# Optimization experiments

Hardware: AMD Instinct MI355X
Metric: run time of the kernel (lower is better)

The kernel has to match this reference:

```python
import jax, jax.numpy as jnp
import numpy as np


def setup_inputs() -> dict:
    key = jax.random.key(0)
    ks = jax.random.split(key, 8)
    B, N, D, H = 8, 512, 64, 64
    user_embeddings = jax.random.normal(ks[0], (B, N, D), dtype=jnp.float32)
    past_lengths = jax.random.randint(ks[1], (B,), 0, N)
    valid_mask = jnp.ones((B, N), dtype=jnp.float32)
    # MLP params: Linear(4D -> H), PReLU (single slope), Linear(H -> 1)
    s1 = 1.0 / np.sqrt(4 * D)
    s2 = 1.0 / np.sqrt(H)
    W1 = jax.random.uniform(ks[2], (H, 4 * D), minval=-s1, maxval=s1, dtype=jnp.float32)
    b1 = jax.random.uniform(ks[3], (H,), minval=-s1, maxval=s1, dtype=jnp.float32)
    prelu_a = jnp.float32(0.25)
    W2 = jax.random.uniform(ks[4], (1, H), minval=-s2, maxval=s2, dtype=jnp.float32)
    b2 = jax.random.uniform(ks[5], (1,), minval=-s2, maxval=s2, dtype=jnp.float32)
    return {"past_lengths": past_lengths, "user_embeddings": user_embeddings,
            "valid_mask": valid_mask, "W1": W1, "b1": b1, "prelu_a": prelu_a,
            "W2": W2, "b2": b2}


def reference(past_lengths, user_embeddings, valid_mask, W1, b1, prelu_a, W2, b2):
    # DIN local activation attention with causal mask.
    # Original math: h = W1 @ concat(Q, K, Q-K, Q*K) + b1 per (q,k) pair.
    # Split W1 into its 4 D-sized blocks so the concat tensor [B,N,N,4D] is
    # never materialized; the pairwise hidden [B,N,N,H] is the only big buffer.
    B, N, D = user_embeddings.shape
    Wq, Wk, Wd, Wm = jnp.split(W1, 4, axis=1)  # each [H, D]
    x = user_embeddings
    # Q and (Q-K)'s +Q part -> per-query term; K and (Q-K)'s -K part -> per-key term
    hq = jnp.einsum('bqd,hd->bqh', x, Wq + Wd)          # [B,N,H]
    hk = jnp.einsum('bkd,hd->bkh', x, Wk - Wd)          # [B,N,H]
    hm = jnp.einsum('bqd,bkd,hd->bqkh', x, x, Wm)       # [B,N,N,H] (Q*K term)
    h = hq[:, :, None, :] + hk[:, None, :, :] + hm + b1
    h = jnp.where(h > 0, h, prelu_a * h)                # PReLU
    scores = jnp.einsum('bqkh,h->bqk', h, W2[0]) + b2[0]  # [B,N,N]
    causal = jnp.tril(jnp.ones((N, N), dtype=scores.dtype))
    scores = scores * causal[None, :, :]
    scores = scores * valid_mask[:, None, :]            # key-side padding mask
    encoded = jnp.einsum('bqk,bkd->bqd', scores, x)     # weighted sum (no softmax)
    return encoded
```

## Files before the change

### kernel.cpp

```cpp
#include <hip/hip_runtime.h>

#define NB 8
#define NN 512

#define WS_WMF 0
#define WS_HQ  4096
#define WS_BF  266240
#define WS_XE  528384

typedef float fx4 __attribute__((ext_vector_type(4)));
typedef short sx8 __attribute__((ext_vector_type(8)));
typedef int   ix4 __attribute__((ext_vector_type(4)));

static __device__ inline unsigned short f2bf(float f) {
    unsigned u = __float_as_uint(f);
    return (unsigned short)((u + 0x7FFFu + ((u >> 16) & 1u)) >> 16);
}

__global__ __launch_bounds__(256) void prep(const float* __restrict__ x,
                                            const float* __restrict__ vm,
                                            const float* __restrict__ W1,
                                            const float* __restrict__ b1,
                                            float* __restrict__ ws) {
    const int t = threadIdx.x;
    const int w = t >> 6, lane = t & 63;
    const int n = lane & 15, quad = lane >> 4;
    const int blk = blockIdx.x;
    const int b   = blk >> 3;
    const int tb  = (blk & 7) * 4;
    const int tile = tb + w;

    __shared__ unsigned short lwf[16 * 64 * 8];
    #pragma unroll
    for (int i = 0; i < 4; ++i) {
        int e = t + i * 256;
        int slot = e >> 6, L = e & 63;
        int isK = slot >> 3, ht = (slot >> 1) & 3, half = slot & 1;
        int nn = L & 15, qd = L >> 4;
        int h = ht * 16 + nn, dbase = half * 32 + qd * 8;
        unsigned short u[8];
        #pragma unroll
        for (int j = 0; j < 8; ++j) {
            int d = dbase + j;
            float wq = W1[h * 256 + d];
            float wk = W1[h * 256 + 64 + d];
            float wd = W1[h * 256 + 128 + d];
            u[j] = f2bf(isK ? (wk - wd) : (wq + wd));
        }
        uint4 o;
        o.x = (unsigned)u[0] | ((unsigned)u[1] << 16);
        o.y = (unsigned)u[2] | ((unsigned)u[3] << 16);
        o.z = (unsigned)u[4] | ((unsigned)u[5] << 16);
        o.w = (unsigned)u[6] | ((unsigned)u[7] << 16);
        ((uint4*)lwf)[e] = o;
    }

    if (blk < 2) {
        float* wmf = ws + WS_WMF;
        int e = blk * 256 + t;
        int slot = e >> 6, L = e & 63;
        int ht = slot >> 1, hf = slot & 1;
        int m = L & 15, qd = L >> 4;
        int h = ht * 16 + m;
        int dbase = hf * 32 + qd * 8;
        #pragma unroll
        for (int j = 0; j < 8; ++j)
            wmf[e * 8 + j] = W1[h * 256 + 192 + dbase + j];
    }
    __syncthreads();

    unsigned short* bfp = (unsigned short*)(ws + WS_BF);
    unsigned short* xep = (unsigned short*)(ws + WS_XE);
    float* hqp = ws + WS_HQ;

    sx8 ax0, ax1;
    {
        const float* xp = x + ((b * 512 + tile * 16 + n) * 64 + quad * 8);
        fx4 a0 = *(const fx4*)xp;
        fx4 a1 = *(const fx4*)(xp + 4);
        fx4 a2 = *(const fx4*)(xp + 32);
        fx4 a3 = *(const fx4*)(xp + 36);
        #pragma unroll
        for (int j = 0; j < 4; ++j) {
            ax0[j] = (short)f2bf(a0[j]); ax0[4 + j] = (short)f2bf(a1[j]);
            ax1[j] = (short)f2bf(a2[j]); ax1[4 + j] = (short)f2bf(a3[j]);
        }
    }

    *(uint4*)(bfp + ((((b * 32 + tile) * 4 + 0) * 64 + lane) << 3)) =
        __builtin_bit_cast(uint4, ax0);
    *(uint4*)(bfp + ((((b * 32 + tile) * 4 + 1) * 64 + lane) << 3)) =
        __builtin_bit_cast(uint4, ax1);

    #pragma unroll
    for (int ht = 0; ht < 4; ++ht) {
        sx8 bq0 = *(const sx8*)(lwf + ((ht * 2 + 0) << 9) + lane * 8);
        sx8 bq1 = *(const sx8*)(lwf + ((ht * 2 + 1) << 9) + lane * 8);
        sx8 bk0 = *(const sx8*)(lwf + ((8 + ht * 2 + 0) << 9) + lane * 8);
        sx8 bk1 = *(const sx8*)(lwf + ((8 + ht * 2 + 1) << 9) + lane * 8);

        float bv = b1[ht * 16 + n];
        fx4 hqa = (fx4){bv, bv, bv, bv};
        hqa = __builtin_amdgcn_mfma_f32_16x16x32_bf16(ax0, bq0, hqa, 0, 0, 0);
        hqa = __builtin_amdgcn_mfma_f32_16x16x32_bf16(ax1, bq1, hqa, 0, 0, 0);
        fx4 hka = (fx4){0.f, 0.f, 0.f, 0.f};
        hka = __builtin_amdgcn_mfma_f32_16x16x32_bf16(ax0, bk0, hka, 0, 0, 0);
        hka = __builtin_amdgcn_mfma_f32_16x16x32_bf16(ax1, bk1, hka, 0, 0, 0);

        #pragma unroll
        for (int r = 0; r < 4; ++r)
            hqp[(b * 512 + tile * 16 + quad * 4 + r) * 64 + ht * 16 + n] = hqa[r];

        int c   = 2 + (ht >> 1);
        int qd2 = (((ht & 1) * 16 + n) >> 3);
        int j   = n & 7;
        #pragma unroll
        for (int r = 0; r < 4; ++r) {
            int nn = quad * 4 + r;
            bfp[((((b * 32 + tile) * 4 + c) * 64 + (qd2 * 16 + nn)) << 3) + j] =
                f2bf(hka[r]);
        }
    }

    #pragma unroll 1
    for (int i = 0; i < 4; ++i) {
        int t5 = tb + i;
        int c32 = t5 >> 1, half = t5 & 1;
        int nt = t >> 6, r = t & 63;
        int L = half * 32 + (r & 31);
        int j0 = (r >> 5) * 4;
        int qd3 = L >> 4, nn3 = L & 15;
        unsigned short u[4];
        #pragma unroll
        for (int ii = 0; ii < 4; ++ii) {
            int key = c32 * 32 + qd3 * 8 + j0 + ii;
            float v = x[(b * 512 + key) * 64 + nt * 16 + nn3] * vm[b * 512 + key];
            u[ii] = f2bf(v);
        }
        uint2 o;
        o.x = (unsigned)u[0] | ((unsigned)u[1] << 16);
        o.y = (unsigned)u[2] | ((unsigned)u[3] << 16);
        *(uint2*)(xep + (((((b * 16 + c32) * 4 + nt) * 64 + L) << 3) + j0)) = o;
    }
}

__global__ __launch_bounds__(256, 2) void k3(const float* __restrict__ x,
                                             const float* __restrict__ prelu_a,
                                             const float* __restrict__ W2,
                                             const float* __restrict__ b2,
                                             const float* __restrict__ ws,
                                             float* __restrict__ out) {
    const int tid  = threadIdx.x;
    const int lane = tid & 63;
    const int w    = tid >> 6;
    const int blk  = blockIdx.x;
    const int m    = blk >> 8;
    const int b    = (blk >> 5) & 7;
    const int s    = blk & 31;
    const int qsel = w >> 1;
    const int h    = w & 1;
    const int band = qsel ? (15 - m) : m;
    const int q    = band * 32 + s;
    const int bq   = b * 512 + q;
    const int cmax = band;
    const int n    = lane & 15, quad = lane >> 4;

    const float* wmf = ws + WS_WMF;
    const float* hq  = ws + WS_HQ;
    const unsigned short* bfp = (const unsigned short*)(ws + WS_BF);
    const unsigned short* xep = (const unsigned short*)(ws + WS_XE);

    const float pa  = prelu_a[0];
    const float b2v = b2[0];

    __shared__ unsigned strip[4][16];
    __shared__ float red[4][64];

    fx4 w2v[4];
    #pragma unroll
    for (int ht = 0; ht < 4; ++ht)
        w2v[ht] = *(const fx4*)(W2 + ht * 16 + quad * 4);
    sx8 oh[4];
    #pragma unroll
    for (int ht = 0; ht < 4; ++ht) {
        sx8 a;
        #pragma unroll
        for (int jj = 0; jj < 8; ++jj) {
            int hp = (ht >> 1) * 32 + quad * 8 + jj;
            a[jj] = (hp == ht * 16 + n) ? (short)0x3F80 : (short)0;
        }
        oh[ht] = a;
    }
    const unsigned sel = (quad < 2) ? 0x05040100u : 0x07060302u;

    fx4 hqv[4];
    #pragma unroll
    for (int ht = 0; ht < 4; ++ht)
        hqv[ht] = *(const fx4*)(hq + bq * 64 + ht * 16 + quad * 4);
    float xq[2][8];
    {
        const float* xp = x + bq * 64 + quad * 8;
        fx4 t0 = *(const fx4*)xp;
        fx4 t1 = *(const fx4*)(xp + 4);
        fx4 t2 = *(const fx4*)(xp + 32);
        fx4 t3 = *(const fx4*)(xp + 36);
        #pragma unroll
        for (int jj = 0; jj < 4; ++jj) {
            xq[0][jj] = t0[jj]; xq[0][4 + jj] = t1[jj];
            xq[1][jj] = t2[jj]; xq[1][4 + jj] = t3[jj];
        }
    }
    sx8 afrag[4][2];
    #pragma unroll
    for (int ht = 0; ht < 4; ++ht)
        #pragma unroll
        for (int hf = 0; hf < 2; ++hf) {
            const float* wp = wmf + (((ht * 2 + hf) * 64 + lane) << 3);
            fx4 w0 = *(const fx4*)wp;
            fx4 w1 = *(const fx4*)(wp + 4);
            sx8 a;
            #pragma unroll
            for (int jj = 0; jj < 4; ++jj) {
                a[jj]     = (short)f2bf(w0[jj] * xq[hf][jj]);
                a[4 + jj] = (short)f2bf(w1[jj] * xq[hf][4 + jj]);
            }
            afrag[ht][hf] = a;
        }

    fx4 eacc[4];
    #pragma unroll
    for (int nt = 0; nt < 4; ++nt) eacc[nt] = (fx4){0.f, 0.f, 0.f, 0.f};

    #pragma unroll 1
    for (int c = h; c <= cmax; c += 2) {
        const unsigned short* ls = bfp + ((((b * 32 + 2 * c) * 4) * 64 + lane) << 3);
        sx8 fa0 = *(const sx8*)(ls);
        sx8 fa1 = *(const sx8*)(ls + 512);
        sx8 fa2 = *(const sx8*)(ls + 1024);
        sx8 fa3 = *(const sx8*)(ls + 1536);
        sx8 fb0 = *(const sx8*)(ls + 2048);
        sx8 fb1 = *(const sx8*)(ls + 2560);
        sx8 fb2 = *(const sx8*)(ls + 3072);
        sx8 fb3 = *(const sx8*)(ls + 3584);
        const unsigned short* le = xep + ((((b * 16 + c) * 4) * 64 + lane) << 3);
        sx8 e0 = *(const sx8*)(le);
        sx8 e1 = *(const sx8*)(le + 512);
        sx8 e2 = *(const sx8*)(le + 1024);
        sx8 e3 = *(const sx8*)(le + 1536);

        fx4 accA[4], accB[4];
        #pragma unroll
        for (int ht = 0; ht < 4; ++ht) { accA[ht] = hqv[ht]; accB[ht] = hqv[ht]; }
        #pragma unroll
        for (int ht = 0; ht < 4; ++ht) {
            accA[ht] = __builtin_amdgcn_mfma_f32_16x16x32_bf16(afrag[ht][0], fa0, accA[ht], 0, 0, 0);
            accB[ht] = __builtin_amdgcn_mfma_f32_16x16x32_bf16(afrag[ht][0], fb0, accB[ht], 0, 0, 0);
        }
        #pragma unroll
        for (int ht = 0; ht < 4; ++ht) {
            accA[ht] = __builtin_amdgcn_mfma_f32_16x16x32_bf16(afrag[ht][1], fa1, accA[ht], 0, 0, 0);
            accB[ht] = __builtin_amdgcn_mfma_f32_16x16x32_bf16(afrag[ht][1], fb1, accB[ht], 0, 0, 0);
        }
        #pragma unroll
        for (int ht = 0; ht < 4; ++ht) {
            accA[ht] = __builtin_amdgcn_mfma_f32_16x16x32_bf16(oh[ht], (ht < 2) ? fa2 : fa3, accA[ht], 0, 0, 0);
            accB[ht] = __builtin_amdgcn_mfma_f32_16x16x32_bf16(oh[ht], (ht < 2) ? fb2 : fb3, accB[ht], 0, 0, 0);
        }

        fx4 s0v = (fx4){0.f, 0.f, 0.f, 0.f};
        fx4 s1v = (fx4){0.f, 0.f, 0.f, 0.f};
        #pragma unroll
        for (int ht = 0; ht < 4; ++ht) {
            fx4 za = accA[ht], zb = accB[ht];
            fx4 ta = __builtin_elementwise_max(za, za * pa);
            fx4 tb = __builtin_elementwise_max(zb, zb * pa);
            s0v = ta * w2v[ht] + s0v;
            s1v = tb * w2v[ht] + s1v;
        }
        float s0 = (s0v[0] + s0v[1]) + (s0v[2] + s0v[3]);
        float s1 = (s1v[0] + s1v[1]) + (s1v[2] + s1v[3]);
        s0 += __shfl_xor(s0, 16, 64);
        s0 += __shfl_xor(s0, 32, 64);
        s1 += __shfl_xor(s1, 16, 64);
        s1 += __shfl_xor(s1, 32, 64);
        int k0 = c * 32 + n;
        s0 = (k0 <= q)      ? s0 + b2v : 0.f;
        s1 = (k0 + 16 <= q) ? s1 + b2v : 0.f;

        unsigned packed = (unsigned)f2bf(s0) | ((unsigned)f2bf(s1) << 16);
        if (quad == 0) strip[w][n] = packed;
        const unsigned* sp = &strip[w][(quad & 1) * 8];
        uint4 wv0 = *(const uint4*)sp;
        uint4 wv1 = *(const uint4*)(sp + 4);
        ix4 sw_;
        sw_[0] = (int)__builtin_amdgcn_perm(wv0.y, wv0.x, sel);
        sw_[1] = (int)__builtin_amdgcn_perm(wv0.w, wv0.z, sel);
        sw_[2] = (int)__builtin_amdgcn_perm(wv1.y, wv1.x, sel);
        sw_[3] = (int)__builtin_amdgcn_perm(wv1.w, wv1.z, sel);
        sx8 sfrag = __builtin_bit_cast(sx8, sw_);

        eacc[0] = __builtin_amdgcn_mfma_f32_16x16x32_bf16(sfrag, e0, eacc[0], 0, 0, 0);
        eacc[1] = __builtin_amdgcn_mfma_f32_16x16x32_bf16(sfrag, e1, eacc[1], 0, 0, 0);
        eacc[2] = __builtin_amdgcn_mfma_f32_16x16x32_bf16(sfrag, e2, eacc[2], 0, 0, 0);
        eacc[3] = __builtin_amdgcn_mfma_f32_16x16x32_bf16(sfrag, e3, eacc[3], 0, 0, 0);
    }

    float ov = eacc[0][0];
    if (quad == 1) ov = eacc[1][0];
    if (quad == 2) ov = eacc[2][0];
    if (quad == 3) ov = eacc[3][0];
    red[w][lane] = ov;
    __syncthreads();

    if (tid < 128) {
        int qs  = tid >> 6;
        int d   = tid & 63;
        int bnd = qs ? (15 - m) : m;
        int bqo = b * 512 + bnd * 32 + s;
        out[bqo * 64 + d] = red[qs * 2][d] + red[qs * 2 + 1][d];
    }
}

extern "C" void kernel_launch(void* const* d_in, const int* in_sizes, int n_in,
                              void* d_out, int out_size, void* d_ws, size_t ws_size,
                              hipStream_t stream) {
    const float* x   = (const float*)d_in[1];
    const float* vmk = (const float*)d_in[2];
    const float* W1  = (const float*)d_in[3];
    const float* b1  = (const float*)d_in[4];
    const float* pa  = (const float*)d_in[5];
    const float* W2  = (const float*)d_in[6];
    const float* b2  = (const float*)d_in[7];
    float* ws  = (float*)d_ws;
    float* out = (float*)d_out;

    hipLaunchKernelGGL(prep, dim3(64), dim3(256), 0, stream, x, vmk, W1, b1, ws);
    hipLaunchKernelGGL(k3, dim3(2048), dim3(256), 0, stream,
                       x, pa, W2, b2, ws, out);
}
```

Baseline: 110.2 us.

## Split score and encode kernels, stage key tiles in LDS with async double-buffered loads

Result: faster. 105.0 us (-4.7%).

```diff
diff --git a/kernel.cpp b/kernel.cpp
--- a/kernel.cpp
+++ b/kernel.cpp
@@ -7,6 +7,7 @@
 #define WS_HQ  4096
 #define WS_BF  266240
 #define WS_XE  528384
+#define WS_SCR 659456
 
 typedef float fx4 __attribute__((ext_vector_type(4)));
 typedef short sx8 __attribute__((ext_vector_type(8)));
@@ -15,6 +16,12 @@
 static __device__ inline unsigned short f2bf(float f) {
     unsigned u = __float_as_uint(f);
     return (unsigned short)((u + 0x7FFFu + ((u >> 16) & 1u)) >> 16);
+}
+
+static __device__ inline void async_cp16(const void* g, void* l) {
+    __builtin_amdgcn_global_load_lds(
+        (const __attribute__((address_space(1))) unsigned int*)g,
+        (__attribute__((address_space(3))) unsigned int*)l, 16, 0, 0);
 }
 
 __global__ __launch_bounds__(256) void prep(const float* __restrict__ x,
@@ -54,7 +61,6 @@
         o.w = (unsigned)u[6] | ((unsigned)u[7] << 16);
         ((uint4*)lwf)[e] = o;
     }
-
     if (blk < 2) {
         float* wmf = ws + WS_WMF;
         int e = blk * 256 + t;
@@ -86,7 +92,6 @@
             ax1[j] = (short)f2bf(a2[j]); ax1[4 + j] = (short)f2bf(a3[j]);
         }
     }
-
     *(uint4*)(bfp + ((((b * 32 + tile) * 4 + 0) * 64 + lane) << 3)) =
         __builtin_bit_cast(uint4, ax0);
     *(uint4*)(bfp + ((((b * 32 + tile) * 4 + 1) * 64 + lane) << 3)) =
@@ -144,59 +149,44 @@
     }
 }
 
-__global__ __launch_bounds__(256, 2) void k3(const float* __restrict__ x,
-                                             const float* __restrict__ prelu_a,
-                                             const float* __restrict__ W2,
-                                             const float* __restrict__ b2,
-                                             const float* __restrict__ ws,
-                                             float* __restrict__ out) {
+__global__ __launch_bounds__(256, 4) void k_score(const float* __restrict__ x,
+                                                  const float* __restrict__ prelu_a,
+                                                  const float* __restrict__ W2,
+                                                  const float* __restrict__ b2,
+                                                  float* __restrict__ ws) {
     const int tid  = threadIdx.x;
     const int lane = tid & 63;
+    const int blk  = blockIdx.x;
+    const int band = (int)((0x4501763298DCABEFULL >> ((blk >> 6) << 2)) & 0xF);
+    const int rest = blk & 63;
+    const int b    = rest >> 3;
+    const int s    = rest & 7;
     const int w    = tid >> 6;
-    const int blk  = blockIdx.x;
-    const int m    = blk >> 8;
-    const int b    = (blk >> 5) & 7;
-    const int s    = blk & 31;
-    const int qsel = w >> 1;
-    const int h    = w & 1;
-    const int band = qsel ? (15 - m) : m;
-    const int q    = band * 32 + s;
+    const int n    = lane & 15, quad = lane >> 4;
+    const int q    = band * 32 + s * 4 + w;
     const int bq   = b * 512 + q;
     const int cmax = band;
-    const int n    = lane & 15, quad = lane >> 4;
 
     const float* wmf = ws + WS_WMF;
     const float* hq  = ws + WS_HQ;
     const unsigned short* bfp = (const unsigned short*)(ws + WS_BF);
-    const unsigned short* xep = (const unsigned short*)(ws + WS_XE);
+    unsigned* scr = (unsigned*)(ws + WS_SCR);
 
     const float pa  = prelu_a[0];
     const float b2v = b2[0];
 
-    __shared__ unsigned strip[4][16];
-    __shared__ float red[4][64];
+    __shared__ uint4 bufS[2][512];
 
     fx4 w2v[4];
     #pragma unroll
     for (int ht = 0; ht < 4; ++ht)
         w2v[ht] = *(const fx4*)(W2 + ht * 16 + quad * 4);
-    sx8 oh[4];
-    #pragma unroll
-    for (int ht = 0; ht < 4; ++ht) {
-        sx8 a;
-        #pragma unroll
-        for (int jj = 0; jj < 8; ++jj) {
-            int hp = (ht >> 1) * 32 + quad * 8 + jj;
-            a[jj] = (hp == ht * 16 + n) ? (short)0x3F80 : (short)0;
-        }
-        oh[ht] = a;
-    }
-    const unsigned sel = (quad < 2) ? 0x05040100u : 0x07060302u;
 
     fx4 hqv[4];
     #pragma unroll
     for (int ht = 0; ht < 4; ++ht)
         hqv[ht] = *(const fx4*)(hq + bq * 64 + ht * 16 + quad * 4);
+
     float xq[2][8];
     {
         const float* xp = x + bq * 64 + quad * 8;
@@ -227,26 +217,35 @@
             afrag[ht][hf] = a;
         }
 
-    fx4 eacc[4];
-    #pragma unroll
-    for (int nt = 0; nt < 4; ++nt) eacc[nt] = (fx4){0.f, 0.f, 0.f, 0.f};
+    int hkoff[4];
+    #pragma unroll
+    for (int ht = 0; ht < 4; ++ht)
+        hkoff[ht] = (2 + (ht >> 1)) * 512 +
+                    (((ht * 2 + (quad >> 1)) & 3) * 16 + n) * 8 + (quad & 1) * 4;
+
+    {
+        const uint4* sS = (const uint4*)(bfp + (unsigned)(b * 32) * 2048);
+        async_cp16(sS + tid,       &bufS[0][tid]);
+        async_cp16(sS + tid + 256, &bufS[0][tid + 256]);
+    }
+    __syncthreads();
 
     #pragma unroll 1
-    for (int c = h; c <= cmax; c += 2) {
-        const unsigned short* ls = bfp + ((((b * 32 + 2 * c) * 4) * 64 + lane) << 3);
+    for (int c = 0; c <= cmax; ++c) {
+        if (c < cmax) {
+            const int p2 = (c + 1) & 1;
+            const uint4* sS = (const uint4*)(bfp + (unsigned)(b * 32 + 2 * (c + 1)) * 2048);
+            async_cp16(sS + tid,       &bufS[p2][tid]);
+            async_cp16(sS + tid + 256, &bufS[p2][tid + 256]);
+        }
+
+        const int p = c & 1;
+        const unsigned short* hb = (const unsigned short*)&bufS[p][0];
+        const unsigned short* ls = hb + lane * 8;
         sx8 fa0 = *(const sx8*)(ls);
         sx8 fa1 = *(const sx8*)(ls + 512);
-        sx8 fa2 = *(const sx8*)(ls + 1024);
-        sx8 fa3 = *(const sx8*)(ls + 1536);
         sx8 fb0 = *(const sx8*)(ls + 2048);
         sx8 fb1 = *(const sx8*)(ls + 2560);
-        sx8 fb2 = *(const sx8*)(ls + 3072);
-        sx8 fb3 = *(const sx8*)(ls + 3584);
-        const unsigned short* le = xep + ((((b * 16 + c) * 4) * 64 + lane) << 3);
-        sx8 e0 = *(const sx8*)(le);
-        sx8 e1 = *(const sx8*)(le + 512);
-        sx8 e2 = *(const sx8*)(le + 1024);
-        sx8 e3 = *(const sx8*)(le + 1536);
 
         fx4 accA[4], accB[4];
         #pragma unroll
@@ -261,17 +260,23 @@
             accA[ht] = __builtin_amdgcn_mfma_f32_16x16x32_bf16(afrag[ht][1], fa1, accA[ht], 0, 0, 0);
             accB[ht] = __builtin_amdgcn_mfma_f32_16x16x32_bf16(afrag[ht][1], fb1, accB[ht], 0, 0, 0);
         }
-        #pragma unroll
-        for (int ht = 0; ht < 4; ++ht) {
-            accA[ht] = __builtin_amdgcn_mfma_f32_16x16x32_bf16(oh[ht], (ht < 2) ? fa2 : fa3, accA[ht], 0, 0, 0);
-            accB[ht] = __builtin_amdgcn_mfma_f32_16x16x32_bf16(oh[ht], (ht < 2) ? fb2 : fb3, accB[ht], 0, 0, 0);
-        }
 
         fx4 s0v = (fx4){0.f, 0.f, 0.f, 0.f};
         fx4 s1v = (fx4){0.f, 0.f, 0.f, 0.f};
         #pragma unroll
         for (int ht = 0; ht < 4; ++ht) {
-            fx4 za = accA[ht], zb = accB[ht];
+            uint2 ha = *(const uint2*)(hb + hkoff[ht]);
+            uint2 hbv = *(const uint2*)(hb + hkoff[ht] + 2048);
+            fx4 hka = (fx4){__uint_as_float(ha.x << 16),
+                            __uint_as_float(ha.x & 0xFFFF0000u),
+                            __uint_as_float(ha.y << 16),
+                            __uint_as_float(ha.y & 0xFFFF0000u)};
+            fx4 hkb = (fx4){__uint_as_float(hbv.x << 16),
+                            __uint_as_float(hbv.x & 0xFFFF0000u),
+                            __uint_as_float(hbv.y << 16),
+                            __uint_as_float(hbv.y & 0xFFFF0000u)};
+            fx4 za = accA[ht] + hka;
+            fx4 zb = accB[ht] + hkb;
             fx4 ta = __builtin_elementwise_max(za, za * pa);
             fx4 tb = __builtin_elementwise_max(zb, zb * pa);
             s0v = ta * w2v[ht] + s0v;
@@ -288,8 +293,35 @@
         s1 = (k0 + 16 <= q) ? s1 + b2v : 0.f;
 
         unsigned packed = (unsigned)f2bf(s0) | ((unsigned)f2bf(s1) << 16);
-        if (quad == 0) strip[w][n] = packed;
-        const unsigned* sp = &strip[w][(quad & 1) * 8];
+        if (quad == 0) scr[(bq << 8) + (c << 4) + n] = packed;
+
+        __syncthreads();
+    }
+}
+
+__global__ __launch_bounds__(256) void k_enc(const float* __restrict__ ws_c,
+                                             float* __restrict__ out) {
+    const int tid  = threadIdx.x;
+    const int lane = tid & 63;
+    const int wid  = blockIdx.x * 4 + (tid >> 6);
+    const int b    = wid >> 9;
+    const int rr   = wid & 511;
+    const int q    = (rr & 1) ? (511 - (rr >> 1)) : (rr >> 1);
+    const int bq   = b * 512 + q;
+    const int n    = lane & 15, quad = lane >> 4;
+
+    const unsigned* scr = (const unsigned*)(ws_c + WS_SCR);
+    const unsigned short* xep = (const unsigned short*)(ws_c + WS_XE);
+    const unsigned sel = (quad < 2) ? 0x05040100u : 0x07060302u;
+
+    fx4 eacc[4];
+    #pragma unroll
+    for (int nt = 0; nt < 4; ++nt) eacc[nt] = (fx4){0.f, 0.f, 0.f, 0.f};
+
+    const int cmax = q >> 5;
+    #pragma unroll 1
+    for (int c = 0; c <= cmax; ++c) {
+        const unsigned* sp = scr + (bq << 8) + (c << 4) + (quad & 1) * 8;
         uint4 wv0 = *(const uint4*)sp;
         uint4 wv1 = *(const uint4*)(sp + 4);
         ix4 sw_;
@@ -299,6 +331,12 @@
         sw_[3] = (int)__builtin_amdgcn_perm(wv1.w, wv1.z, sel);
         sx8 sfrag = __builtin_bit_cast(sx8, sw_);
 
+        const unsigned short* le = xep + ((((b * 16 + c) * 4) * 64 + lane) << 3);
+        sx8 e0 = *(const sx8*)(le);
+        sx8 e1 = *(const sx8*)(le + 512);
+        sx8 e2 = *(const sx8*)(le + 1024);
+        sx8 e3 = *(const sx8*)(le + 1536);
+
         eacc[0] = __builtin_amdgcn_mfma_f32_16x16x32_bf16(sfrag, e0, eacc[0], 0, 0, 0);
         eacc[1] = __builtin_amdgcn_mfma_f32_16x16x32_bf16(sfrag, e1, eacc[1], 0, 0, 0);
         eacc[2] = __builtin_amdgcn_mfma_f32_16x16x32_bf16(sfrag, e2, eacc[2], 0, 0, 0);
@@ -309,16 +347,7 @@
     if (quad == 1) ov = eacc[1][0];
     if (quad == 2) ov = eacc[2][0];
     if (quad == 3) ov = eacc[3][0];
-    red[w][lane] = ov;
-    __syncthreads();
-
-    if (tid < 128) {
-        int qs  = tid >> 6;
-        int d   = tid & 63;
-        int bnd = qs ? (15 - m) : m;
-        int bqo = b * 512 + bnd * 32 + s;
-        out[bqo * 64 + d] = red[qs * 2][d] + red[qs * 2 + 1][d];
-    }
+    out[bq * 64 + quad * 16 + n] = ov;
 }
 
 extern "C" void kernel_launch(void* const* d_in, const int* in_sizes, int n_in,
@@ -335,6 +364,7 @@
     float* out = (float*)d_out;
 
     hipLaunchKernelGGL(prep, dim3(64), dim3(256), 0, stream, x, vmk, W1, b1, ws);
-    hipLaunchKernelGGL(k3, dim3(2048), dim3(256), 0, stream,
-                       x, pa, W2, b2, ws, out);
-}
+    hipLaunchKernelGGL(k_score, dim3(1024), dim3(256), 0, stream,
+                       x, pa, W2, b2, ws);
+    hipLaunchKernelGGL(k_enc, dim3(1024), dim3(256), 0, stream, ws, out);
+}
```
